# Kernel optimization log

Hardware: AMD Instinct MI355X
Metric: run time of the kernel (lower is better)

Reference implementation:

```python
import jax, jax.numpy as jnp
import numpy as np

B, N, H, HEADS, PH, VD = 32, 256, 768, 12, 128, 16
DH = H // HEADS
VOCAB = 2 * VD + 3


def layer_norm(x, g, b, eps=1e-5):
    m = jnp.mean(x, axis=-1, keepdims=True)
    v = jnp.mean((x - m) ** 2, axis=-1, keepdims=True)
    return (x - m) * jax.lax.rsqrt(v + eps) * g + b


def setup_inputs() -> dict:
    key = jax.random.key(0)
    ks = jax.random.split(key, 12)
    # clamped relative-distance index pool, as in PathEmbeddingDistance
    t = np.arange(N)
    pool = t[None, :] - t[:, None]
    pool = np.clip(pool, -VD - 1, VD + 1) + VD + 1  # in [0, 2*VD+2]
    s = 0.02
    return {
        "nodes": jax.random.normal(ks[0], (B, N, H), jnp.float32),
        "bias": jnp.zeros((B, 1, 1, N), jnp.float32),
        "path_pool": jnp.asarray(pool, jnp.int32),
        "pos_table": jax.random.normal(ks[1], (VOCAB, PH), jnp.float32) * s,
        "Wq": jax.random.normal(ks[2], (H, H), jnp.float32) * s, "bq": jnp.zeros((H,), jnp.float32),
        "Wk": jax.random.normal(ks[3], (H, H), jnp.float32) * s, "bk": jnp.zeros((H,), jnp.float32),
        "Wv": jax.random.normal(ks[4], (H, H), jnp.float32) * s, "bv": jnp.zeros((H,), jnp.float32),
        "Wsk": jax.random.normal(ks[5], (PH, DH), jnp.float32) * s, "bsk": jnp.zeros((DH,), jnp.float32),
        "Wsv": jax.random.normal(ks[6], (PH, DH), jnp.float32) * s, "bsv": jnp.zeros((DH,), jnp.float32),
        "Wo": jax.random.normal(ks[7], (H, H), jnp.float32) * s, "bo": jnp.zeros((H,), jnp.float32),
        "g_path": jnp.ones((PH,), jnp.float32), "b_path": jnp.zeros((PH,), jnp.float32),
        "g_norm": jnp.ones((H,), jnp.float32), "b_norm": jnp.zeros((H,), jnp.float32),
    }


def reference(nodes, bias, path_pool, pos_table, Wq, bq, Wk, bk, Wv, bv,
              Wsk, bsk, Wsv, bsv, Wo, bo, g_path, b_path, g_norm, b_norm):
    # path embedding lookup (batch-independent: torch expand == broadcast)
    paths = pos_table[path_pool]                      # (N, N, PH)
    paths = layer_norm(paths, g_path, b_path)
    q = (nodes @ Wq + bq).reshape(B, N, HEADS, DH).transpose(0, 2, 1, 3)
    k = (nodes @ Wk + bk).reshape(B, N, HEADS, DH).transpose(0, 2, 1, 3)
    v = (nodes @ Wv + bv).reshape(B, N, HEADS, DH).transpose(0, 2, 1, 3)
    struct_k = paths @ Wsk + bsk                      # (N, N, DH)
    struct_v = paths @ Wsv + bsv                      # (N, N, DH)
    q = q * (DH ** -0.5)
    w = jnp.einsum("bhid,bhjd->bhij", q, k)
    struct_w = jnp.einsum("bhid,ijd->bhij", q, struct_k)
    w = jax.nn.softmax(w + struct_w + bias, axis=-1)  # (B, HEADS, N, N)
    out = jnp.einsum("bhij,bhjd->bhid", w, v) + jnp.einsum("bhij,ijd->bhid", w, struct_v)
    out = out.transpose(0, 2, 1, 3).reshape(B, N, H)  # combine heads
    out = jax.nn.relu(out @ Wo + bo)
    return layer_norm(nodes + out, g_norm, b_norm), w
```

## Files before the change

kernel.cpp:

```cpp
#include <hip/hip_runtime.h>
#include <hip/hip_bf16.h>

#define BB 32
#define NN 256
#define HH 768
#define NHEADS 12
#define DH 64
#define PHDIM 128
#define NVOCAB 35

typedef short bf16x8 __attribute__((ext_vector_type(8)));
typedef float f32x16 __attribute__((ext_vector_type(16)));
typedef unsigned u32x2 __attribute__((ext_vector_type(2)));

#define MFMA32 __builtin_amdgcn_mfma_f32_32x32x16_bf16

__device__ __forceinline__ unsigned short f2bf(float f) {
    unsigned u = __float_as_uint(f);
    unsigned r = (u + 0x7fffu + ((u >> 16) & 1u)) >> 16;
    return (unsigned short)r;
}

__device__ __forceinline__ float bf2f(unsigned short b) {
    return __uint_as_float(((unsigned)b) << 16);
}

__device__ __forceinline__ unsigned pk2(float a, float b) {
    return (unsigned)f2bf(a) | ((unsigned)f2bf(b) << 16);
}

__device__ __forceinline__ bf16x8 pack8(const float f[8]) {
    bf16x8 r;
#pragma unroll
    for (int e = 0; e < 8; ++e) r[e] = (short)f2bf(f[e]);
    return r;
}

__global__ __launch_bounds__(256) void k_prep(
        const float* __restrict__ nodes, unsigned short* __restrict__ nodes_bf,
        const float* __restrict__ Wq, const float* __restrict__ Wk,
        const float* __restrict__ Wv, const float* __restrict__ Wo,
        unsigned short* __restrict__ Wt,
        const float* __restrict__ pos_table,
        const float* __restrict__ g_path, const float* __restrict__ b_path,
        const float* __restrict__ Wsk, const float* __restrict__ bsk,
        const float* __restrict__ Wsv, const float* __restrict__ bsv,
        unsigned short* __restrict__ skv_bf, unsigned short* __restrict__ svv_t_bf) {
    const int blk = blockIdx.x;
    const int tid = threadIdx.x;

    if (blk < 6144) {
        int i = (blk * 256 + tid) * 4;
        float4 v = *reinterpret_cast<const float4*>(&nodes[i]);
        ushort4 o;
        o.x = f2bf(v.x); o.y = f2bf(v.y); o.z = f2bf(v.z); o.w = f2bf(v.w);
        *reinterpret_cast<ushort4*>(&nodes_bf[i]) = o;
        return;
    }

    if (blk < 6720) {
        __shared__ unsigned short tile[64][72];
        int wb = blk - 6144;
        int z = wb / 144;
        int rem = wb - z * 144;
        int k0 = (rem / 12) * 64, c0 = (rem % 12) * 64;
        const float* W = (z == 0) ? Wq : (z == 1) ? Wk : (z == 2) ? Wv : Wo;
        unsigned short* out = Wt + (size_t)z * HH * HH;
#pragma unroll
        for (int l = 0; l < 16; ++l) {
            int e = tid + l * 256;
            int r = e >> 6, c = e & 63;
            tile[c][r] = f2bf(W[(size_t)(k0 + r) * HH + c0 + c]);
        }
        __syncthreads();
#pragma unroll
        for (int l = 0; l < 2; ++l) {
            int e = tid + l * 256;
            int c = e >> 3, ch = e & 7;
            *reinterpret_cast<bf16x8*>(&out[(size_t)(c0 + c) * HH + k0 + ch * 8]) =
                *reinterpret_cast<const bf16x8*>(&tile[c][ch * 8]);
        }
        return;
    }

    {
        int v = blk - 6720;
        int t = tid;
        if (v >= NVOCAB) {
            if (t < 64) skv_bf[v * 64 + t] = 0;
            else if (t < 128 && v < 48) svv_t_bf[(t - 64) * 48 + v] = 0;
            return;
        }
        __shared__ float x[PHDIM];
        __shared__ float red[PHDIM];
        float xv = 0.f;
        if (t < PHDIM) { xv = pos_table[v * PHDIM + t]; red[t] = xv; }
        __syncthreads();
        for (int s = 64; s > 0; s >>= 1) { if (t < s) red[t] += red[t + s]; __syncthreads(); }
        float mean = red[0] / PHDIM;
        __syncthreads();
        if (t < PHDIM) { float c = xv - mean; red[t] = c * c; }
        __syncthreads();
        for (int s = 64; s > 0; s >>= 1) { if (t < s) red[t] += red[t + s]; __syncthreads(); }
        float var = red[0] / PHDIM;
        __syncthreads();
        if (t < PHDIM) x[t] = (xv - mean) * rsqrtf(var + 1e-5f) * g_path[t] + b_path[t];
        __syncthreads();
        if (t < 64) {
            float acc = bsk[t];
            for (int p = 0; p < PHDIM; ++p) acc += x[p] * Wsk[p * DH + t];
            skv_bf[v * 64 + t] = f2bf(acc);
        } else if (t < 128) {
            int d = t - 64;
            float acc = bsv[d];
            for (int p = 0; p < PHDIM; ++p) acc += x[p] * Wsv[p * DH + d];
            svv_t_bf[d * 48 + v] = f2bf(acc);
        }
    }
}

__global__ __launch_bounds__(256) void k_qkv(
        const unsigned short* __restrict__ Abf, const unsigned short* __restrict__ Wt,
        const float* __restrict__ bq, const float* __restrict__ bk, const float* __restrict__ bv,
        unsigned short* __restrict__ q_bf, unsigned short* __restrict__ k_bf,
        unsigned short* __restrict__ v_bf_t) {
    __shared__ __align__(16) char smem_raw[34816];
    unsigned short (*Al)[128 * 32] = reinterpret_cast<unsigned short(*)[128 * 32]>(smem_raw);
    unsigned short (*Bl)[128 * 32] = reinterpret_cast<unsigned short(*)[128 * 32]>(smem_raw + 16384);
    unsigned short (*vstage)[136]  = reinterpret_cast<unsigned short(*)[136]>(smem_raw);

    const int tid = threadIdx.x;
    const int w = tid >> 6, lane = tid & 63;
    const int il = lane & 31, hi = lane >> 5;
    const int wr = w >> 1, wc = w & 1;
    const int rowBase = blockIdx.x * 128;
    const int colBase = blockIdx.y * 128;
    const int sel = colBase / HH;
    const int jjBase0 = colBase - sel * HH;
    const float* bias = (sel == 0) ? bq : (sel == 1) ? bk : bv;

    f32x16 acc[2][2] = {};

    auto STAGE = [&](int buf, int k0) {
#pragma unroll
        for (int c = 0; c < 2; ++c) {
            int e = tid + c * 256;
            int row = e >> 2;
            int cb = (e & 3) << 4;
            int sc = cb ^ (((row >> 1) & 3) << 4);
            __builtin_amdgcn_global_load_lds(
                (const __attribute__((address_space(1))) unsigned int*)(Abf + (size_t)(rowBase + row) * HH + k0 + (sc >> 1)),
                (__attribute__((address_space(3))) unsigned int*)(&Al[buf][row * 32 + (cb >> 1)]), 16, 0, 0);
            __builtin_amdgcn_global_load_lds(
                (const __attribute__((address_space(1))) unsigned int*)(Wt + (size_t)(colBase + row) * HH + k0 + (sc >> 1)),
                (__attribute__((address_space(3))) unsigned int*)(&Bl[buf][row * 32 + (cb >> 1)]), 16, 0, 0);
        }
    };

    STAGE(0, 0);
    __syncthreads();
    for (int t = 0; t < 24; ++t) {
        int buf = t & 1;
        if (t < 23) STAGE(buf ^ 1, (t + 1) * 32);
#pragma unroll
        for (int ks = 0; ks < 2; ++ks) {
            bf16x8 af[2], bfr[2];
            int cb = (ks << 5) + (hi << 4);
#pragma unroll
            for (int t2 = 0; t2 < 2; ++t2) {
                int rrow = wr * 64 + t2 * 32 + il;
                af[t2] = *reinterpret_cast<const bf16x8*>(
                    &Al[buf][rrow * 32 + ((cb ^ (((rrow >> 1) & 3) << 4)) >> 1)]);
                int crow = wc * 64 + t2 * 32 + il;
                bfr[t2] = *reinterpret_cast<const bf16x8*>(
                    &Bl[buf][crow * 32 + ((cb ^ (((crow >> 1) & 3) << 4)) >> 1)]);
            }
            acc[0][0] = MFMA32(af[0], bfr[0], acc[0][0], 0, 0, 0);
            acc[0][1] = MFMA32(af[0], bfr[1], acc[0][1], 0, 0, 0);
            acc[1][0] = MFMA32(af[1], bfr[0], acc[1][0], 0, 0, 0);
            acc[1][1] = MFMA32(af[1], bfr[1], acc[1][1], 0, 0, 0);
        }
        __syncthreads();
    }

    if (sel < 2) {
        unsigned short* outp = (sel == 0) ? q_bf : k_bf;
        float scale = (sel == 0) ? 0.125f : 1.0f;
        unsigned short* qst = &vstage[0][0];
        const int b = rowBase >> 8;
        const int hB = jjBase0 >> 6;
#pragma unroll
        for (int rt = 0; rt < 2; ++rt)
#pragma unroll
            for (int ct = 0; ct < 2; ++ct) {
                int jjB = jjBase0 + wc * 64 + ct * 32;
                float bias_v = bias[jjB + il];
#pragma unroll
                for (int r = 0; r < 16; ++r) {
                    int ir = (r & 3) + 8 * (r >> 2) + 4 * hi;
                    qst[(w * 32 + ir) * 34 + il] = f2bf((acc[rt][ct][r] + bias_v) * scale);
                }
                int R0 = rowBase + wr * 64 + rt * 32;
                int t32 = (R0 & 255) >> 5;
                int bh = b * NHEADS + hB + wc;
#pragma unroll
                for (int g = 0; g < 2; ++g) {
                    int kt = ct * 2 + g;
                    size_t base = ((size_t)(bh * 8 + t32) * 4 + kt) * 512;
                    bf16x8 vv = *reinterpret_cast<const bf16x8*>(
                        &qst[(w * 32 + (lane & 31)) * 34 + g * 16 + (lane >> 5) * 8]);
                    *reinterpret_cast<bf16x8*>(&outp[base + lane * 8]) = vv;
                }
            }
    } else {
#pragma unroll
        for (int rt = 0; rt < 2; ++rt)
#pragma unroll
            for (int ct = 0; ct < 2; ++ct) {
                int jjB = jjBase0 + wc * 64 + ct * 32;
                float bias_v = bias[jjB + il];
#pragma unroll
                for (int r = 0; r < 16; ++r) {
                    int rl = wr * 64 + rt * 32 + ((r & 3) + 8 * (r >> 2) + 4 * hi);
                    vstage[wc * 64 + ct * 32 + il][rl] = f2bf(acc[rt][ct][r] + bias_v);
                }
            }
        __syncthreads();
        int b = rowBase >> 8, n0 = rowBase & 255;
        int h0v = jjBase0 >> 6;
#pragma unroll
        for (int q = 0; q < 8; ++q) {
            int rid = w * 8 + q;
            int head = rid >> 4, jtl = (rid >> 2) & 3, ks = (rid >> 1) & 1, dh = rid & 1;
            int bh = b * NHEADS + h0v + head;
            int jtg = (n0 >> 5) + jtl;
            size_t base = ((((size_t)(bh * 8 + jtg) * 2 + ks) * 2 + dh) * 64) * 8;
            bf16x8 vv = *reinterpret_cast<const bf16x8*>(
                &vstage[head * 64 + dh * 32 + (lane & 31)][jtl * 32 + ks * 16 + (lane >> 5) * 8]);
            *reinterpret_cast<bf16x8*>(&v_bf_t[base + lane * 8]) = vv;
        }
    }
}

__global__ __launch_bounds__(256, 4) void k_attn(
        const unsigned short* __restrict__ q_bf, const unsigned short* __restrict__ k_bf,
        const unsigned short* __restrict__ v_bf_t,
        const unsigned short* __restrict__ skv_bf, const unsigned short* __restrict__ svv_t_bf,
        const float* __restrict__ bias,
        float* __restrict__ wout, unsigned short* __restrict__ attn_out) {
    __shared__ __align__(16) float qs_s[32][36];
    __shared__ __align__(16) float wsum[32][48];
    __shared__ __align__(16) float oex[3][32][68];
    __shared__ float msum[4][32][2];
    __shared__ float bias_s[NN];

    const int bx0 = blockIdx.x;
    const int bx = (bx0 & 7) * 384 + (bx0 >> 3);
    const int bh = bx >> 3, rowblk = bx & 7;
    const int b = bh / NHEADS, h = bh - b * NHEADS;
    const int tid = threadIdx.x;
    const int w = tid >> 6, lane = tid & 63;
    const int il = lane & 31, hi = lane >> 5;
    const int i0 = rowblk * 32;
    const int ig = i0 + il;

    bias_s[tid] = bias[b * NN + tid];
#pragma unroll
    for (int z = 0; z < 6; ++z) ((float*)wsum)[tid + z * 256] = 0.f;

    bf16x8 qf[4];
#pragma unroll
    for (int kt = 0; kt < 4; ++kt)
        qf[kt] = *reinterpret_cast<const bf16x8*>(
            &q_bf[((((size_t)bh * 8 + rowblk) * 4 + kt) * 64 + lane) * 8]);

    if (w == 0) {
        f32x16 qa0 = {}, qa1 = {};
#pragma unroll
        for (int kt = 0; kt < 4; ++kt) {
            bf16x8 s0 = *reinterpret_cast<const bf16x8*>(&skv_bf[(size_t)il * 64 + kt * 16 + 8 * hi]);
            bf16x8 s1 = *reinterpret_cast<const bf16x8*>(&skv_bf[(size_t)(32 + il) * 64 + kt * 16 + 8 * hi]);
            qa0 = MFMA32(qf[kt], s0, qa0, 0, 0, 0);
            qa1 = MFMA32(qf[kt], s1, qa1, 0, 0, 0);
        }
#pragma unroll
        for (int r = 0; r < 16; ++r) {
            int ir = (r & 3) + 8 * (r >> 2) + 4 * hi;
            qs_s[ir][il] = qa0[r];
            if (il < 3) qs_s[ir][32 + il] = qa1[r];
        }
    }

    f32x16 S[2] = {};
    __builtin_amdgcn_s_setprio(1);
#pragma unroll
    for (int jt = 0; jt < 2; ++jt) {
        int jtg = w * 2 + jt;
#pragma unroll
        for (int kt = 0; kt < 4; ++kt) {
            bf16x8 kf = *reinterpret_cast<const bf16x8*>(
                &k_bf[((((size_t)bh * 8 + jtg) * 4 + kt) * 64 + lane) * 8]);
            S[jt] = MFMA32(kf, qf[kt], S[jt], 0, 0, 0);
        }
    }
    __builtin_amdgcn_s_setprio(0);

    __syncthreads();

    const int jb = w * 64;
    {
        float qlo = qs_s[il][0], qhi = qs_s[il][34];
#pragma unroll
        for (int jt = 0; jt < 2; ++jt) {
#pragma unroll
            for (int rg = 0; rg < 4; ++rg) {
                int j0 = jb + jt * 32 + rg * 8 + 4 * hi;
                float4 bv4 = *reinterpret_cast<const float4*>(&bias_s[j0]);
                float bvf[4] = {bv4.x, bv4.y, bv4.z, bv4.w};
#pragma unroll
                for (int e = 0; e < 4; ++e) {
                    int dd = j0 + e - ig;
                    float sw = (dd < -16) ? qlo : (dd > 16) ? qhi : qs_s[il][dd + 17];
                    S[jt][rg * 4 + e] += bvf[e] + sw;
                }
            }
        }
    }

    float m = -3.4e38f;
#pragma unroll
    for (int jt = 0; jt < 2; ++jt)
#pragma unroll
        for (int r = 0; r < 16; ++r) m = fmaxf(m, S[jt][r]);
    m = fmaxf(m, __shfl_xor(m, 32));
    float sum = 0.f;
#pragma unroll
    for (int jt = 0; jt < 2; ++jt)
#pragma unroll
        for (int r = 0; r < 16; ++r) { float p = __expf(S[jt][r] - m); S[jt][r] = p; sum += p; }
    sum += __shfl_xor(sum, 32);
    if (hi == 0) { msum[w][il][0] = m; msum[w][il][1] = sum; }
    __syncthreads();

    {
        float m0 = msum[0][il][0], m1 = msum[1][il][0];
        float m2 = msum[2][il][0], m3 = msum[3][il][0];
        float M = fmaxf(fmaxf(m0, m1), fmaxf(m2, m3));
        float sumT = msum[0][il][1] * __expf(m0 - M) + msum[1][il][1] * __expf(m1 - M) +
                     msum[2][il][1] * __expf(m2 - M) + msum[3][il][1] * __expf(m3 - M);
        float scale = __expf(m - M) / sumT;
#pragma unroll
        for (int jt = 0; jt < 2; ++jt)
#pragma unroll
            for (int r = 0; r < 16; ++r) S[jt][r] *= scale;
    }

#pragma unroll
    for (int jt = 0; jt < 2; ++jt) {
#pragma unroll
        for (int rg = 0; rg < 4; ++rg) {
            float4 val;
            val.x = S[jt][rg * 4 + 0];
            val.y = S[jt][rg * 4 + 1];
            val.z = S[jt][rg * 4 + 2];
            val.w = S[jt][rg * 4 + 3];
            *reinterpret_cast<float4*>(
                &wout[((size_t)(bh * NN + ig)) * NN + jb + jt * 32 + rg * 8 + 4 * hi]) = val;
        }
    }

    {
        float elo = 0.f, ehi = 0.f;
#pragma unroll
        for (int jt = 0; jt < 2; ++jt)
#pragma unroll
            for (int r = 0; r < 16; ++r) {
                int j = jb + jt * 32 + (r & 3) + 8 * (r >> 2) + 4 * hi;
                int dd = j - ig;
                float p = S[jt][r];
                if (dd < -16) elo += p;
                else if (dd > 16) ehi += p;
                else wsum[il][dd + 17] = p;
            }
        if (elo != 0.f) atomicAdd(&wsum[il][0], elo);
        if (ehi != 0.f) atomicAdd(&wsum[il][34], ehi);
    }

    f32x16 O0 = {}, O1 = {};
    __builtin_amdgcn_s_setprio(1);
#pragma unroll
    for (int jt = 0; jt < 2; ++jt) {
        int jtg = w * 2 + jt;
#pragma unroll
        for (int ks = 0; ks < 2; ++ks) {
            unsigned w0 = pk2(S[jt][8 * ks + 0], S[jt][8 * ks + 1]);
            unsigned w1 = pk2(S[jt][8 * ks + 2], S[jt][8 * ks + 3]);
            unsigned w2 = pk2(S[jt][8 * ks + 4], S[jt][8 * ks + 5]);
            unsigned w3 = pk2(S[jt][8 * ks + 6], S[jt][8 * ks + 7]);
            unsigned s0 = hi ? w0 : w2, s1 = hi ? w1 : w3;
            unsigned y0 = (unsigned)__shfl_xor((int)s0, 32);
            unsigned y1 = (unsigned)__shfl_xor((int)s1, 32);
            union { bf16x8 v; unsigned u[4]; } Bf;
            Bf.u[0] = hi ? y0 : w0;
            Bf.u[1] = hi ? y1 : w1;
            Bf.u[2] = hi ? w2 : y0;
            Bf.u[3] = hi ? w3 : y1;
            bf16x8 va0 = *reinterpret_cast<const bf16x8*>(
                &v_bf_t[(((((size_t)bh * 8 + jtg) * 2 + ks) * 2 + 0) * 64 + lane) * 8]);
            bf16x8 va1 = *reinterpret_cast<const bf16x8*>(
                &v_bf_t[(((((size_t)bh * 8 + jtg) * 2 + ks) * 2 + 1) * 64 + lane) * 8]);
            O0 = MFMA32(va0, Bf.v, O0, 0, 0, 0);
            O1 = MFMA32(va1, Bf.v, O1, 0, 0, 0);
        }
    }
    __builtin_amdgcn_s_setprio(0);

    if (w != 0) {
#pragma unroll
        for (int qq = 0; qq < 4; ++qq) {
            int d0 = 8 * qq + 4 * hi;
            *reinterpret_cast<float4*>(&oex[w - 1][il][d0]) =
                float4{O0[4 * qq + 0], O0[4 * qq + 1], O0[4 * qq + 2], O0[4 * qq + 3]};
            *reinterpret_cast<float4*>(&oex[w - 1][il][32 + d0]) =
                float4{O1[4 * qq + 0], O1[4 * qq + 1], O1[4 * qq + 2], O1[4 * qq + 3]};
        }
    }
    __syncthreads();

    if (w == 0) {
#pragma unroll
        for (int s = 0; s < 3; ++s) {
#pragma unroll
            for (int qq = 0; qq < 4; ++qq) {
                int d0 = 8 * qq + 4 * hi;
                float4 p0 = *reinterpret_cast<const float4*>(&oex[s][il][d0]);
                float4 p1 = *reinterpret_cast<const float4*>(&oex[s][il][32 + d0]);
                O0[4 * qq + 0] += p0.x; O0[4 * qq + 1] += p0.y;
                O0[4 * qq + 2] += p0.z; O0[4 * qq + 3] += p0.w;
                O1[4 * qq + 0] += p1.x; O1[4 * qq + 1] += p1.y;
                O1[4 * qq + 2] += p1.z; O1[4 * qq + 3] += p1.w;
            }
        }

#pragma unroll
        for (int kt = 0; kt < 3; ++kt) {
            float4 a0 = *reinterpret_cast<const float4*>(&wsum[il][kt * 16 + 8 * hi]);
            float4 a1 = *reinterpret_cast<const float4*>(&wsum[il][kt * 16 + 8 * hi + 4]);
            float af[8] = {a0.x, a0.y, a0.z, a0.w, a1.x, a1.y, a1.z, a1.w};
            bf16x8 Bf = pack8(af);
            bf16x8 sa0 = *reinterpret_cast<const bf16x8*>(&svv_t_bf[(size_t)il * 48 + kt * 16 + 8 * hi]);
            bf16x8 sa1 = *reinterpret_cast<const bf16x8*>(&svv_t_bf[(size_t)(32 + il) * 48 + kt * 16 + 8 * hi]);
            O0 = MFMA32(sa0, Bf, O0, 0, 0, 0);
            O1 = MFMA32(sa1, Bf, O1, 0, 0, 0);
        }

#pragma unroll
        for (int qq = 0; qq < 4; ++qq) {
            int d0 = 8 * qq + 4 * hi;
            u32x2 o0, o1;
            o0[0] = pk2(O0[4 * qq + 0], O0[4 * qq + 1]);
            o0[1] = pk2(O0[4 * qq + 2], O0[4 * qq + 3]);
            o1[0] = pk2(O1[4 * qq + 0], O1[4 * qq + 1]);
            o1[1] = pk2(O1[4 * qq + 2], O1[4 * qq + 3]);
            size_t base = ((size_t)(b * NN + i0 + il)) * HH + h * 64;
            *reinterpret_cast<u32x2*>(&attn_out[base + d0]) = o0;
            *reinterpret_cast<u32x2*>(&attn_out[base + 32 + d0]) = o1;
        }
    }
}

__global__ __launch_bounds__(256) void k_ogemm(
        const unsigned short* __restrict__ Abf, const unsigned short* __restrict__ Bt,
        const float* __restrict__ bo, unsigned short* __restrict__ Cout) {
    __shared__ unsigned short Al[2][128 * 32];
    __shared__ unsigned short Bl[2][128 * 32];

    const int tid = threadIdx.x;
    const int w = tid >> 6, lane = tid & 63;
    const int il = lane & 31, hi = lane >> 5;
    const int wr = w >> 1, wc = w & 1;
    const int rowBase = blockIdx.x * 128;
    const int colBase = blockIdx.y * 128;

    f32x16 acc[2][2] = {};

    auto STAGE = [&](int buf, int k0) {
#pragma unroll
        for (int c = 0; c < 2; ++c) {
            int e = tid + c * 256;
            int row = e >> 2;
            int cb = (e & 3) << 4;
            int sc = cb ^ (((row >> 1) & 3) << 4);
            __builtin_amdgcn_global_load_lds(
                (const __attribute__((address_space(1))) unsigned int*)(Abf + (size_t)(rowBase + row) * HH + k0 + (sc >> 1)),
                (__attribute__((address_space(3))) unsigned int*)(&Al[buf][row * 32 + (cb >> 1)]), 16, 0, 0);
            __builtin_amdgcn_global_load_lds(
                (const __attribute__((address_space(1))) unsigned int*)(Bt + (size_t)(colBase + row) * HH + k0 + (sc >> 1)),
                (__attribute__((address_space(3))) unsigned int*)(&Bl[buf][row * 32 + (cb >> 1)]), 16, 0, 0);
        }
    };

    STAGE(0, 0);
    __syncthreads();
    for (int t = 0; t < 24; ++t) {
        int buf = t & 1;
        if (t < 23) STAGE(buf ^ 1, (t + 1) * 32);
#pragma unroll
        for (int ks = 0; ks < 2; ++ks) {
            bf16x8 af[2], bfr[2];
            int cb = (ks << 5) + (hi << 4);
#pragma unroll
            for (int t2 = 0; t2 < 2; ++t2) {
                int rrow = wr * 64 + t2 * 32 + il;
                af[t2] = *reinterpret_cast<const bf16x8*>(
                    &Al[buf][rrow * 32 + ((cb ^ (((rrow >> 1) & 3) << 4)) >> 1)]);
                int crow = wc * 64 + t2 * 32 + il;
                bfr[t2] = *reinterpret_cast<const bf16x8*>(
                    &Bl[buf][crow * 32 + ((cb ^ (((crow >> 1) & 3) << 4)) >> 1)]);
            }
            acc[0][0] = MFMA32(af[0], bfr[0], acc[0][0], 0, 0, 0);
            acc[0][1] = MFMA32(af[0], bfr[1], acc[0][1], 0, 0, 0);
            acc[1][0] = MFMA32(af[1], bfr[0], acc[1][0], 0, 0, 0);
            acc[1][1] = MFMA32(af[1], bfr[1], acc[1][1], 0, 0, 0);
        }
        __syncthreads();
    }

#pragma unroll
    for (int rt = 0; rt < 2; ++rt)
#pragma unroll
        for (int ct = 0; ct < 2; ++ct) {
            int col = colBase + wc * 64 + ct * 32 + il;
            float bias_v = bo[col];
#pragma unroll
            for (int r = 0; r < 16; ++r) {
                int row = rowBase + wr * 64 + rt * 32 + ((r & 3) + 8 * (r >> 2) + 4 * hi);
                Cout[(size_t)row * HH + col] = f2bf(fmaxf(acc[rt][ct][r] + bias_v, 0.f));
            }
        }
}

__global__ __launch_bounds__(256) void k_ln(
        const unsigned short* __restrict__ nodes_bf, const unsigned short* __restrict__ proj,
        const float* __restrict__ g, const float* __restrict__ bta,
        float* __restrict__ out) {
    __shared__ float red[2][4];
    int row = blockIdx.x;
    int tid = threadIdx.x;
    int w = tid >> 6, lane = tid & 63;
    float x[3];
    float s = 0.f, s2 = 0.f;
#pragma unroll
    for (int l = 0; l < 3; ++l) {
        int c = tid + l * 256;
        x[l] = bf2f(nodes_bf[(size_t)row * HH + c]) + bf2f(proj[(size_t)row * HH + c]);
        s += x[l];
        s2 += x[l] * x[l];
    }
#pragma unroll
    for (int off = 32; off > 0; off >>= 1) {
        s += __shfl_xor(s, off);
        s2 += __shfl_xor(s2, off);
    }
    if (lane == 0) { red[0][w] = s; red[1][w] = s2; }
    __syncthreads();
    float ts = red[0][0] + red[0][1] + red[0][2] + red[0][3];
    float ts2 = red[1][0] + red[1][1] + red[1][2] + red[1][3];
    float mean = ts / HH;
    float var = ts2 / HH - mean * mean;
    float inv = rsqrtf(fmaxf(var, 0.f) + 1e-5f);
#pragma unroll
    for (int l = 0; l < 3; ++l) {
        int c = tid + l * 256;
        out[(size_t)row * HH + c] = (x[l] - mean) * inv * g[c] + bta[c];
    }
}

extern "C" void kernel_launch(void* const* d_in, const int* in_sizes, int n_in,
                              void* d_out, int out_size, void* d_ws, size_t ws_size,
                              hipStream_t stream) {
    const float* nodes     = (const float*)d_in[0];
    const float* bias      = (const float*)d_in[1];
    const float* pos_table = (const float*)d_in[3];
    const float* Wq = (const float*)d_in[4];  const float* bq = (const float*)d_in[5];
    const float* Wk = (const float*)d_in[6];  const float* bk = (const float*)d_in[7];
    const float* Wv = (const float*)d_in[8];  const float* bv = (const float*)d_in[9];
    const float* Wsk = (const float*)d_in[10]; const float* bsk = (const float*)d_in[11];
    const float* Wsv = (const float*)d_in[12]; const float* bsv = (const float*)d_in[13];
    const float* Wo = (const float*)d_in[14]; const float* bo = (const float*)d_in[15];
    const float* g_path = (const float*)d_in[16]; const float* b_path = (const float*)d_in[17];
    const float* g_norm = (const float*)d_in[18]; const float* b_norm = (const float*)d_in[19];

    float* out0 = (float*)d_out;
    float* wout = out0 + (size_t)BB * NN * HH;

    const size_t per = (size_t)BB * NN * HH;
    char* p = (char*)d_ws;
    unsigned short* q_bf    = (unsigned short*)p; p += per * 2;
    unsigned short* k_bf    = (unsigned short*)p; p += per * 2;
    unsigned short* v_bf_t  = (unsigned short*)p; p += per * 2;
    unsigned short* skv_bf  = (unsigned short*)p; p += 64 * 64 * 2;
    unsigned short* svv_t   = (unsigned short*)p; p += 64 * 48 * 2;
    unsigned short* nodes_bf= (unsigned short*)p; p += per * 2;
    unsigned short* Wt      = (unsigned short*)p; p += (size_t)4 * HH * HH * 2;
    unsigned short* attn_bf = (unsigned short*)p; p += per * 2;
    unsigned short* proj_bf = v_bf_t;

    k_prep<<<6784, 256, 0, stream>>>(nodes, nodes_bf, Wq, Wk, Wv, Wo, Wt,
                                     pos_table, g_path, b_path, Wsk, bsk, Wsv, bsv,
                                     skv_bf, svv_t);

    dim3 g2(64, 18);
    k_qkv<<<g2, 256, 0, stream>>>(nodes_bf, Wt, bq, bk, bv, q_bf, k_bf, v_bf_t);

    k_attn<<<BB * NHEADS * 8, 256, 0, stream>>>(q_bf, k_bf, v_bf_t, skv_bf, svv_t, bias, wout, attn_bf);

    dim3 g4(64, 6);
    k_ogemm<<<g4, 256, 0, stream>>>(attn_bf, Wt + (size_t)3 * HH * HH, bo, proj_bf);

    k_ln<<<BB * NN, 256, 0, stream>>>(nodes_bf, proj_bf, g_norm, b_norm, out0);
}
```

Measured before the change: 136.1 us.

## Shrink attention LDS via bf16 partial exchange, raise occupancy, defer weight stores

```diff
diff --git a/kernel.cpp b/kernel.cpp
--- a/kernel.cpp
+++ b/kernel.cpp
@@ -119,7 +119,7 @@
     }
 }
 
-__global__ __launch_bounds__(256) void k_qkv(
+__global__ __launch_bounds__(256, 4) void k_qkv(
         const unsigned short* __restrict__ Abf, const unsigned short* __restrict__ Wt,
         const float* __restrict__ bq, const float* __restrict__ bk, const float* __restrict__ bv,
         unsigned short* __restrict__ q_bf, unsigned short* __restrict__ k_bf,
@@ -242,7 +242,7 @@
     }
 }
 
-__global__ __launch_bounds__(256, 4) void k_attn(
+__global__ __launch_bounds__(256, 6) void k_attn(
         const unsigned short* __restrict__ q_bf, const unsigned short* __restrict__ k_bf,
         const unsigned short* __restrict__ v_bf_t,
         const unsigned short* __restrict__ skv_bf, const unsigned short* __restrict__ svv_t_bf,
@@ -250,7 +250,7 @@
         float* __restrict__ wout, unsigned short* __restrict__ attn_out) {
     __shared__ __align__(16) float qs_s[32][36];
     __shared__ __align__(16) float wsum[32][48];
-    __shared__ __align__(16) float oex[3][32][68];
+    __shared__ __align__(8) unsigned oex[3][32][36];
     __shared__ float msum[4][32][2];
     __shared__ float bias_s[NN];
 
@@ -353,20 +353,6 @@
         for (int jt = 0; jt < 2; ++jt)
 #pragma unroll
             for (int r = 0; r < 16; ++r) S[jt][r] *= scale;
-    }
-
-#pragma unroll
-    for (int jt = 0; jt < 2; ++jt) {
-#pragma unroll
-        for (int rg = 0; rg < 4; ++rg) {
-            float4 val;
-            val.x = S[jt][rg * 4 + 0];
-            val.y = S[jt][rg * 4 + 1];
-            val.z = S[jt][rg * 4 + 2];
-            val.w = S[jt][rg * 4 + 3];
-            *reinterpret_cast<float4*>(
-                &wout[((size_t)(bh * NN + ig)) * NN + jb + jt * 32 + rg * 8 + 4 * hi]) = val;
-        }
     }
 
     {
@@ -415,14 +401,31 @@
     }
     __builtin_amdgcn_s_setprio(0);
 
+#pragma unroll
+    for (int jt = 0; jt < 2; ++jt) {
+#pragma unroll
+        for (int rg = 0; rg < 4; ++rg) {
+            float4 val;
+            val.x = S[jt][rg * 4 + 0];
+            val.y = S[jt][rg * 4 + 1];
+            val.z = S[jt][rg * 4 + 2];
+            val.w = S[jt][rg * 4 + 3];
+            *reinterpret_cast<float4*>(
+                &wout[((size_t)(bh * NN + ig)) * NN + jb + jt * 32 + rg * 8 + 4 * hi]) = val;
+        }
+    }
+
     if (w != 0) {
 #pragma unroll
         for (int qq = 0; qq < 4; ++qq) {
             int d0 = 8 * qq + 4 * hi;
-            *reinterpret_cast<float4*>(&oex[w - 1][il][d0]) =
-                float4{O0[4 * qq + 0], O0[4 * qq + 1], O0[4 * qq + 2], O0[4 * qq + 3]};
-            *reinterpret_cast<float4*>(&oex[w - 1][il][32 + d0]) =
-                float4{O1[4 * qq + 0], O1[4 * qq + 1], O1[4 * qq + 2], O1[4 * qq + 3]};
+            u32x2 p0, p1;
+            p0[0] = pk2(O0[4 * qq + 0], O0[4 * qq + 1]);
+            p0[1] = pk2(O0[4 * qq + 2], O0[4 * qq + 3]);
+            p1[0] = pk2(O1[4 * qq + 0], O1[4 * qq + 1]);
+            p1[1] = pk2(O1[4 * qq + 2], O1[4 * qq + 3]);
+            *reinterpret_cast<u32x2*>(&oex[w - 1][il][d0 >> 1]) = p0;
+            *reinterpret_cast<u32x2*>(&oex[w - 1][il][(32 + d0) >> 1]) = p1;
         }
     }
     __syncthreads();
@@ -433,12 +436,16 @@
 #pragma unroll
             for (int qq = 0; qq < 4; ++qq) {
                 int d0 = 8 * qq + 4 * hi;
-                float4 p0 = *reinterpret_cast<const float4*>(&oex[s][il][d0]);
-                float4 p1 = *reinterpret_cast<const float4*>(&oex[s][il][32 + d0]);
-                O0[4 * qq + 0] += p0.x; O0[4 * qq + 1] += p0.y;
-                O0[4 * qq + 2] += p0.z; O0[4 * qq + 3] += p0.w;
-                O1[4 * qq + 0] += p1.x; O1[4 * qq + 1] += p1.y;
-                O1[4 * qq + 2] += p1.z; O1[4 * qq + 3] += p1.w;
+                u32x2 p0 = *reinterpret_cast<const u32x2*>(&oex[s][il][d0 >> 1]);
+                u32x2 p1 = *reinterpret_cast<const u32x2*>(&oex[s][il][(32 + d0) >> 1]);
+                O0[4 * qq + 0] += __uint_as_float((p0[0] & 0xffffu) << 16);
+                O0[4 * qq + 1] += __uint_as_float(p0[0] & 0xffff0000u);
+                O0[4 * qq + 2] += __uint_as_float((p0[1] & 0xffffu) << 16);
+                O0[4 * qq + 3] += __uint_as_float(p0[1] & 0xffff0000u);
+                O1[4 * qq + 0] += __uint_as_float((p1[0] & 0xffffu) << 16);
+                O1[4 * qq + 1] += __uint_as_float(p1[0] & 0xffff0000u);
+                O1[4 * qq + 2] += __uint_as_float((p1[1] & 0xffffu) << 16);
+                O1[4 * qq + 3] += __uint_as_float(p1[1] & 0xffff0000u);
             }
         }
 
```

Result: slower. 171.1 us (+25.7%).
